# Optimization experiments

Measured on AMD Instinct MI355X. Metric: run time of the kernel, lower is better.

## Reference

```python
import jax, jax.numpy as jnp
from jax import lax
import numpy as np

BATCH = 8
FH, FW, A = 32, 256, 6            # feature map height/width, anchors per cell
TOTAL_ANCHORS = FH * FW * A       # 49152
PRE_NMS_TOPN = 2000
POST_NMS_TOPN = 300
NMS_IOU = 0.7
VARIANCES = np.array([0.1, 0.1, 0.2, 0.2], dtype=np.float32)


def _make_anchors():
    # Grid anchors, normalized [y1, x1, y2, x2], A scales/ratios per cell.
    cy = (np.arange(FH, dtype=np.float32) + 0.5) / FH
    cx = (np.arange(FW, dtype=np.float32) + 0.5) / FW
    sizes = np.array([0.02, 0.04, 0.08, 0.03, 0.06, 0.12], dtype=np.float32)  # A sizes
    ratios = np.array([1.0, 1.0, 1.0, 2.0, 0.5, 1.0], dtype=np.float32)
    h = sizes * np.sqrt(ratios)
    w = sizes / np.sqrt(ratios)
    CY, CX = np.meshgrid(cy, cx, indexing='ij')            # [FH, FW]
    CY = CY[:, :, None]; CX = CX[:, :, None]               # [FH, FW, 1]
    y1 = CY - 0.5 * h; x1 = CX - 0.5 * w
    y2 = CY + 0.5 * h; x2 = CX + 0.5 * w
    anc = np.stack([y1, x1, y2, x2], axis=-1).reshape(-1, 4)  # [TOTAL_ANCHORS, 4]
    return jnp.asarray(anc, dtype=jnp.float32)


def setup_inputs() -> dict:
    key = jax.random.key(0)
    k1, k2 = jax.random.split(key)
    rpn_bbox_deltas = jax.random.normal(k1, (BATCH, FH, FW, A * 4), dtype=jnp.float32)
    rpn_labels = jax.random.normal(k2, (BATCH, FH, FW, A), dtype=jnp.float32)
    return {
        'rpn_bbox_deltas': rpn_bbox_deltas,
        'rpn_labels': rpn_labels,
        'anchors': _make_anchors(),
    }


def _decode(anchors, deltas):
    # anchors [N,4] y1x1y2x2, deltas [B,N,4] (dy,dx,dh,dw)
    ah = anchors[:, 2] - anchors[:, 0]
    aw = anchors[:, 3] - anchors[:, 1]
    acy = anchors[:, 0] + 0.5 * ah
    acx = anchors[:, 1] + 0.5 * aw
    bh = jnp.exp(deltas[..., 2]) * ah
    bw = jnp.exp(deltas[..., 3]) * aw
    bcy = deltas[..., 0] * ah + acy
    bcx = deltas[..., 1] * aw + acx
    y1 = bcy - 0.5 * bh
    x1 = bcx - 0.5 * bw
    return jnp.stack([y1, x1, y1 + bh, x1 + bw], axis=-1)


def _pairwise_iou(boxes):
    # boxes [N,4] -> [N,N]
    y1, x1, y2, x2 = boxes[:, 0], boxes[:, 1], boxes[:, 2], boxes[:, 3]
    area = (y2 - y1) * (x2 - x1)
    iy1 = jnp.maximum(y1[:, None], y1[None, :])
    ix1 = jnp.maximum(x1[:, None], x1[None, :])
    iy2 = jnp.minimum(y2[:, None], y2[None, :])
    ix2 = jnp.minimum(x2[:, None], x2[None, :])
    inter = jnp.maximum(iy2 - iy1, 0.0) * jnp.maximum(ix2 - ix1, 0.0)
    union = area[:, None] + area[None, :] - inter
    return inter / jnp.maximum(union, 1e-8)


def _nms_single(boxes, scores):
    # boxes [P,4] sorted by score desc, scores [P] in [0,1]
    P = boxes.shape[0]
    ious = _pairwise_iou(boxes)
    idx = jnp.arange(P)

    def body(i, keep):
        sup = (ious[i] > NMS_IOU) & (idx > i) & keep[i]
        return keep & (~sup)

    keep = lax.fori_loop(0, P, body, jnp.ones((P,), dtype=bool))
    masked = jnp.where(keep, scores, -1.0)
    top_sc, top_idx = lax.top_k(masked, POST_NMS_TOPN)
    valid = top_sc >= 0.0
    out_boxes = jnp.clip(boxes[top_idx], 0.0, 1.0) * valid[:, None].astype(boxes.dtype)
    out_scores = jnp.where(valid, top_sc, 0.0)
    return out_boxes, out_scores


def reference(rpn_bbox_deltas, rpn_labels, anchors):
    B = rpn_bbox_deltas.shape[0]
    deltas = rpn_bbox_deltas.reshape(B, TOTAL_ANCHORS, 4)
    labels = jax.nn.softmax(rpn_labels, axis=-1).reshape(B, TOTAL_ANCHORS)
    deltas = deltas * jnp.asarray(VARIANCES)
    bboxes = _decode(anchors, deltas)                          # [B, N, 4]
    pre_scores, pre_idx = lax.top_k(labels, PRE_NMS_TOPN)      # [B, P]
    pre_boxes = jnp.take_along_axis(bboxes, pre_idx[:, :, None], axis=1)  # [B, P, 4]
    roi_boxes, roi_scores = jax.vmap(_nms_single)(pre_boxes, pre_scores)
    return (lax.stop_gradient(roi_boxes), lax.stop_gradient(roi_scores))
```

## Files before the change

### kernel.cpp

```cpp
#include <hip/hip_runtime.h>
#include <cstdint>
#include <cstddef>

#define BATCH 8
#define FHh   32
#define FWw   256
#define NA    6
#define NANCH (FHh * FWw * NA)
#define PRE_K 2000
#define POST_K 300
#define SEGS  192
#define CAND_CAP 4096
#define BIN_LO 0x3E2Au
#define SH_BASE 0x3E00u
#define SHBIN 512
#define RMAX_EP 20

typedef unsigned long long u64;

#define WS_SC   0
#define WS_HIST 1572864
#define WS_CUTV 3670016
#define WS_CAND 4194304
#define WS_CNT  7340032
#define WS_PB   7602176
#define WS_PS   7858176
#define WS_SUPP 8388608

__global__ __launch_bounds__(1024) void k_zero(uint4* __restrict__ hist4) {
    hist4[threadIdx.x] = make_uint4(0u, 0u, 0u, 0u);
}

__global__ void k_softhist(const float* __restrict__ labels, float* __restrict__ scores,
                           unsigned int* __restrict__ hist) {
    int pos = blockIdx.x * blockDim.x + threadIdx.x;
    if (pos >= BATCH * FHh * FWw) return;
    int b = pos / (FHh * FWw);
    const float2* in2 = (const float2*)(labels + (size_t)pos * NA);
    float v[NA];
    float2 p0 = in2[0], p1 = in2[1], p2 = in2[2];
    v[0] = p0.x; v[1] = p0.y; v[2] = p1.x; v[3] = p1.y; v[4] = p2.x; v[5] = p2.y;
    float m = v[0];
#pragma unroll
    for (int a = 1; a < NA; ++a) m = fmaxf(m, v[a]);
    float s = 0.0f;
#pragma unroll
    for (int a = 0; a < NA; ++a) { v[a] = expf(v[a] - m); s += v[a]; }
    float inv = 1.0f / s;
    float2* o2 = (float2*)(scores + (size_t)pos * NA);
    unsigned int* hb = hist + (size_t)b * SHBIN;
#pragma unroll
    for (int a = 0; a < NA; ++a) v[a] *= inv;
    o2[0] = make_float2(v[0], v[1]);
    o2[1] = make_float2(v[2], v[3]);
    o2[2] = make_float2(v[4], v[5]);
#pragma unroll
    for (int a = 0; a < NA; ++a) {
        unsigned int bin = __float_as_uint(v[a]) >> 16;
        if (bin >= BIN_LO) atomicAdd(&hb[bin - SH_BASE], 1u);
    }
}

__global__ __launch_bounds__(64) void k_sfx(unsigned int* __restrict__ hist,
                                            unsigned int* __restrict__ cutv) {
    const int b = blockIdx.x;
    const int t = threadIdx.x;
    unsigned int* h = hist + (size_t)b * SHBIN;
    const int blk0 = SHBIN - 8 * (t + 1);
    uint4 q0 = *(const uint4*)(h + blk0);
    uint4 q1 = *(const uint4*)(h + blk0 + 4);
    unsigned int hv[8] = {q0.x, q0.y, q0.z, q0.w, q1.x, q1.y, q1.z, q1.w};
    unsigned int s = hv[0] + hv[1] + hv[2] + hv[3] + hv[4] + hv[5] + hv[6] + hv[7];
    unsigned int inc = s;
#pragma unroll
    for (int d = 1; d < 64; d <<= 1) {
        unsigned int v = __shfl_up(inc, d);
        if (t >= d) inc += v;
    }
    unsigned int run = inc - s;
    unsigned int o[8];
#pragma unroll
    for (int g = 7; g >= 0; --g) { o[g] = run; run += hv[g]; }
#pragma unroll
    for (int g = 0; g < 8; ++g)
        if (o[g] < PRE_K && o[g] + hv[g] >= PRE_K)
            cutv[b * 16] = SH_BASE + (unsigned)(blk0 + g);
    uint4 w0 = make_uint4(o[0], o[1], o[2], o[3]);
    uint4 w1 = make_uint4(o[4], o[5], o[6], o[7]);
    *(uint4*)(h + blk0) = w0;
    *(uint4*)(h + blk0 + 4) = w1;
}

__global__ __launch_bounds__(256) void k_gather(
        const float* __restrict__ scores, const unsigned int* __restrict__ cutv,
        u64* __restrict__ cand, unsigned int* __restrict__ counts) {
    const int blk = blockIdx.x;
    const int b = blk / SEGS, kb = blk - b * SEGS;
    const int tid = threadIdx.x;
    __shared__ unsigned int s_cut;
    __shared__ unsigned int s_wcnt[4];
    if (tid == 0) s_cut = cutv[b * 16];
    __syncthreads();
    const int idx = kb * 256 + tid;
    const unsigned int bits = __float_as_uint(scores[(size_t)b * NANCH + idx]);
    const bool pass = (bits >> 16) >= s_cut;
    const u64 m = __ballot(pass);
    const int lane = tid & 63, w = tid >> 6;
    if (lane == 0) s_wcnt[w] = (unsigned int)__popcll(m);
    __syncthreads();
    unsigned int pre = 0, tot = 0;
#pragma unroll
    for (int i = 0; i < 4; ++i) { unsigned int c = s_wcnt[i]; if (i < w) pre += c; tot += c; }
    if (pass) {
        unsigned int rank = pre + (unsigned int)__popcll(m & ((1ull << lane) - 1ull));
        cand[((size_t)b * SEGS + kb) * 256 + rank] =
            ((u64)bits << 32) | (unsigned int)(~idx);
    }
    if (tid == 0) counts[b * SEGS + kb] = tot;
}

__global__ __launch_bounds__(1024) void k_rankdec(
        const u64* __restrict__ cand, const unsigned int* __restrict__ counts,
        const unsigned int* __restrict__ sfx,
        const float* __restrict__ deltas, const float* __restrict__ anchors,
        float4* __restrict__ pre_boxes, float* __restrict__ pre_scores) {
    const int b = blockIdx.x;
    const int tid = threadIdx.x;
    __shared__ u64 grouped[CAND_CAP];
    __shared__ unsigned int cursor[CAND_CAP];
    for (int i = tid; i < CAND_CAP; i += 1024) { grouped[i] = 0ull; cursor[i] = 0u; }
    __syncthreads();
    const unsigned int* sfb = sfx + (size_t)b * SHBIN;

    if (tid < SEGS) {
        unsigned int v = counts[b * SEGS + tid];
        const u64* seg = cand + ((size_t)b * SEGS + tid) * 256;
        for (unsigned int k = 0; k < v; ++k) {
            u64 key = seg[k];
            unsigned int bin = (unsigned int)(key >> 48) - SH_BASE;
            unsigned int g0 = sfb[bin];
            unsigned int slot = g0 + atomicAdd(&cursor[g0], 1u);
            if (slot < CAND_CAP) grouped[slot] = key;
        }
    }
    __syncthreads();

    for (int p = tid; p < CAND_CAP; p += 1024) {
        u64 key = grouped[p];
        if (key == 0ull) continue;
        unsigned int bin = (unsigned int)(key >> 48) - SH_BASE;
        unsigned int g0 = sfb[bin];
        unsigned int c = cursor[g0];
        unsigned int rank = g0;
        unsigned int qe = g0 + c; if (qe > CAND_CAP) qe = CAND_CAP;
        for (unsigned int q = g0; q < qe; ++q) rank += (grouped[q] > key);
        if (rank < PRE_K) {
            int idx = (int)(~(unsigned int)key);
            float score = __uint_as_float((unsigned int)(key >> 32));
            const float* anc = anchors + (size_t)idx * 4;
            const float* del = deltas + ((size_t)b * NANCH + idx) * 4;
            float a0 = anc[0], a1 = anc[1], a2 = anc[2], a3 = anc[3];
            float ah = a2 - a0, aw = a3 - a1;
            float acy = a0 + 0.5f * ah, acx = a1 + 0.5f * aw;
            float d0 = del[0] * 0.1f, d1 = del[1] * 0.1f;
            float d2 = del[2] * 0.2f, d3 = del[3] * 0.2f;
            float bh = expf(d2) * ah, bw = expf(d3) * aw;
            float bcy = d0 * ah + acy, bcx = d1 * aw + acx;
            float y1 = bcy - 0.5f * bh, x1 = bcx - 0.5f * bw;
            pre_boxes[(size_t)b * PRE_K + rank] = make_float4(y1, x1, y1 + bh, x1 + bw);
            pre_scores[(size_t)b * PRE_K + rank] = score;
        }
    }
}

__global__ __launch_bounds__(64) void k_iou(const float4* __restrict__ pre_boxes,
                                            u64* __restrict__ supp) {
    const int cb = blockIdx.x;
    const int rb = blockIdx.y;
    const int b  = blockIdx.z;
    const int lane = threadIdx.x;
    const int i = rb * 64 + lane;
    const int j0 = cb * 64;
    if (cb < rb) return;
    __shared__ float4 sbox[64];
    const float4* boxes = pre_boxes + (size_t)b * PRE_K;
    int j = j0 + lane;
    sbox[lane] = (j < PRE_K) ? boxes[j] : make_float4(0.f, 0.f, 0.f, 0.f);
    __syncthreads();
    if (i >= PRE_K) return;
    float4 bi = boxes[i];
    float area_i = (bi.z - bi.x) * (bi.w - bi.y);
    u64 bits = 0ull;
    const int tmax = (PRE_K - j0 < 64) ? (PRE_K - j0) : 64;
    for (int t = 0; t < tmax; ++t) {
        int jj = j0 + t;
        if (jj <= i) continue;
        float4 bj = sbox[t];
        float iy1 = fmaxf(bi.x, bj.x), ix1 = fmaxf(bi.y, bj.y);
        float iy2 = fminf(bi.z, bj.z), ix2 = fminf(bi.w, bj.w);
        float inter = fmaxf(iy2 - iy1, 0.0f) * fmaxf(ix2 - ix1, 0.0f);
        float area_j = (bj.z - bj.x) * (bj.w - bj.y);
        float uni = area_i + area_j - inter;
        float iou = inter / fmaxf(uni, 1e-8f);
        if (iou > 0.7f) bits |= (1ull << t);
    }
    supp[((size_t)b * PRE_K + i) * 32 + cb] = bits;
}

__device__ __forceinline__ u64 readlane64(u64 x, int ln) {
    unsigned int lo = __builtin_amdgcn_readlane((unsigned int)x, ln);
    unsigned int hi = __builtin_amdgcn_readlane((unsigned int)(x >> 32), ln);
    return ((u64)hi << 32) | (u64)lo;
}

template <int ROWS>
__device__ __forceinline__ u64 proc_epoch(const u64* __restrict__ bufp, int wi,
                                          int p, int w, u64& r0, u64& r1) {
    const u64 wmask = (w >= wi) ? ~0ull : 0ull;
    u64 acc = r0 | r1;
    u64 cur = ~(readlane64(acc, wi) | readlane64(acc, 32 + wi));
#pragma unroll
    for (int g = 0; g < ROWS / 16; ++g) {
        u64 ld[8];
#pragma unroll
        for (int k = 0; k < 8; ++k)
            ld[k] = bufp[(g * 16 + 2 * k + p) * 32 + w] & wmask;
        u64 t0 = (ld[0] | ld[1]) | (ld[2] | ld[3]);
        u64 t1 = (ld[4] | ld[5]) | (ld[6] | ld[7]);
        u64 tor = t0 | t1;
        u64 intra = readlane64(tor, wi) | readlane64(tor, 32 + wi);
        if (intra == 0ull) {
#pragma unroll
            for (int k = 0; k < 8; ++k) {
                int bitpos = g * 16 + 2 * k + p;
                u64 msk = ((cur >> bitpos) & 1ull) ? ~0ull : 0ull;
                if (k & 1) r1 |= ld[k] & msk; else r0 |= ld[k] & msk;
            }
        } else {
#pragma unroll
            for (int c = 0; c < 16; ++c) {
                const int pi = c & 1, k = c >> 1;
                if ((cur >> (g * 16 + c)) & 1ull) {
                    cur &= ~readlane64(ld[k], pi * 32 + wi);
                    u64 msk = (p == pi) ? ~0ull : 0ull;
                    if (k & 1) r1 |= ld[k] & msk; else r0 |= ld[k] & msk;
                }
            }
        }
    }
    return cur;
}

__device__ void fill_epoch(u64* __restrict__ dst, const float4* __restrict__ boxes,
                           int e, int l, int rows) {
    const int total = rows * 32;
    for (int idx = l; idx < total; idx += 64) {
        const int rl = idx >> 5, w = idx & 31;
        const int i = e * 64 + rl;
        const int j0 = w * 64;
        u64 bits = 0ull;
        if (i < PRE_K && j0 + 63 > i) {
            float4 bi = boxes[i];
            float area_i = (bi.z - bi.x) * (bi.w - bi.y);
            const int tmax = (PRE_K - j0 < 64) ? (PRE_K - j0) : 64;
            for (int t = 0; t < tmax; ++t) {
                int jj = j0 + t;
                if (jj <= i) continue;
                float4 bj = boxes[jj];
                float iy1 = fmaxf(bi.x, bj.x), ix1 = fmaxf(bi.y, bj.y);
                float iy2 = fminf(bi.z, bj.z), ix2 = fminf(bi.w, bj.w);
                float inter = fmaxf(iy2 - iy1, 0.0f) * fmaxf(ix2 - ix1, 0.0f);
                float area_j = (bj.z - bj.x) * (bj.w - bj.y);
                float uni = area_i + area_j - inter;
                float iou = inter / fmaxf(uni, 1e-8f);
                if (iou > 0.7f) bits |= (1ull << t);
            }
        }
        dst[idx] = bits;
    }
}

__global__ __launch_bounds__(64) void k_final(const u64* __restrict__ supp,
                        const float4* __restrict__ pre_boxes,
                        const float* __restrict__ pre_scores,
                        float* __restrict__ out) {
    const int b = blockIdx.x;
    const int l = threadIdx.x;
    const int p = l >> 5, w = l & 31;
    float* ob = out + (size_t)b * POST_K * 4;
    float* os = out + (size_t)BATCH * POST_K * 4 + (size_t)b * POST_K;
    for (int t = l; t < POST_K * 4; t += 64) ob[t] = 0.0f;
    for (int t = l; t < POST_K; t += 64) os[t] = 0.0f;
    asm volatile("s_waitcnt vmcnt(0)" ::: "memory");

    __shared__ u64 sbuf[3][2048];
    const char* Sb = (const char*)(supp + (size_t)b * PRE_K * 32);
    const float4* boxes = pre_boxes + (size_t)b * PRE_K;

#define ISSUE_EPOCH(ep)                                                       \
    do {                                                                      \
        const char* gsrc_ = Sb + (size_t)(ep) * 16384 + (size_t)l * 16;       \
        char* ldst_ = (char*)&sbuf[(ep) % 3][0];                              \
        _Pragma("unroll")                                                     \
        for (int k_ = 0; k_ < 16; ++k_)                                       \
            __builtin_amdgcn_global_load_lds(                                 \
                (const __attribute__((address_space(1))) void*)(gsrc_ + k_ * 1024), \
                (__attribute__((address_space(3))) void*)(ldst_ + k_ * 1024), \
                16, 0, 0);                                                    \
    } while (0)

    u64 r0 = 0ull, r1 = 0ull;
    int kept = 0;
    bool done = false;
    ISSUE_EPOCH(0);
    ISSUE_EPOCH(1);
    for (int e = 0; e <= RMAX_EP - 3; ++e) {
        ISSUE_EPOCH(e + 2);
        asm volatile("s_waitcnt vmcnt(32)" ::: "memory");
        __builtin_amdgcn_sched_barrier(0);
        u64 curf = proc_epoch<64>(&sbuf[e % 3][0], e, p, w, r0, r1);
        kept += __builtin_popcountll(curf);
        if (kept >= POST_K) { done = true; break; }
    }
    if (!done) {
        asm volatile("s_waitcnt vmcnt(16)" ::: "memory");
        __builtin_amdgcn_sched_barrier(0);
        u64 curf = proc_epoch<64>(&sbuf[(RMAX_EP - 2) % 3][0], RMAX_EP - 2, p, w, r0, r1);
        kept += __builtin_popcountll(curf);
        if (kept >= POST_K) done = true;
    }
    if (!done) {
        asm volatile("s_waitcnt vmcnt(0)" ::: "memory");
        __builtin_amdgcn_sched_barrier(0);
        u64 curf = proc_epoch<64>(&sbuf[(RMAX_EP - 1) % 3][0], RMAX_EP - 1, p, w, r0, r1);
        kept += __builtin_popcountll(curf);
        if (kept >= POST_K) done = true;
    }
    if (!done) {
        for (int e = RMAX_EP; e < 32; ++e) {
            fill_epoch(&sbuf[0][0], boxes, e, l, (e == 31) ? 16 : 64);
            __syncthreads();
            u64 curf;
            if (e < 31) curf = proc_epoch<64>(&sbuf[0][0], e, p, w, r0, r1);
            else        curf = proc_epoch<16>(&sbuf[0][0], e, p, w, r0, r1) & 0xFFFFull;
            kept += __builtin_popcountll(curf);
            if (kept >= POST_K) break;
            __syncthreads();
        }
    }
    asm volatile("s_waitcnt vmcnt(0)" ::: "memory");
#undef ISSUE_EPOCH

    u64 full = r0 | r1;
    u64 oth = __shfl(full, w + 32);
    u64 kw = ~(full | oth);
    if (w == 31) kw &= 0xFFFFull;
    int cnt = (l < 32) ? __builtin_popcountll(kw) : 0;
    int cum = cnt;
#pragma unroll
    for (int d = 1; d < 64; d <<= 1) {
        int v = __shfl_up(cum, d);
        if (l >= d) cum += v;
    }
    int r = cum - cnt;
    __syncthreads();
    if (l < 32) {
        u64 m = kw;
        while (m != 0ull && r < POST_K) {
            int t = __builtin_ctzll(m);
            m &= m - 1ull;
            int i = w * 64 + t;
            float4 bx = pre_boxes[(size_t)b * PRE_K + i];
            ob[r * 4 + 0] = fminf(fmaxf(bx.x, 0.0f), 1.0f);
            ob[r * 4 + 1] = fminf(fmaxf(bx.y, 0.0f), 1.0f);
            ob[r * 4 + 2] = fminf(fmaxf(bx.z, 0.0f), 1.0f);
            ob[r * 4 + 3] = fminf(fmaxf(bx.w, 0.0f), 1.0f);
            os[r] = pre_scores[(size_t)b * PRE_K + i];
            ++r;
        }
    }
}

extern "C" void kernel_launch(void* const* d_in, const int* in_sizes, int n_in,
                              void* d_out, int out_size, void* d_ws, size_t ws_size,
                              hipStream_t stream) {
    const float* deltas  = (const float*)d_in[0];
    const float* labels  = (const float*)d_in[1];
    const float* anchors = (const float*)d_in[2];
    float* out = (float*)d_out;

    char* ws = (char*)d_ws;
    float* scores          = (float*)(ws + WS_SC);
    unsigned int* hist     = (unsigned int*)(ws + WS_HIST);
    unsigned int* cutv     = (unsigned int*)(ws + WS_CUTV);
    u64* cd                = (u64*)(ws + WS_CAND);
    unsigned int* cntp     = (unsigned int*)(ws + WS_CNT);
    float4* pre_boxes      = (float4*)(ws + WS_PB);
    float* pre_scores      = (float*)(ws + WS_PS);
    u64* sp                = (u64*)(ws + WS_SUPP);

    k_zero<<<1, 1024, 0, stream>>>((uint4*)hist);
    k_softhist<<<(BATCH * FHh * FWw + 255) / 256, 256, 0, stream>>>(labels, scores, hist);
    k_sfx<<<BATCH, 64, 0, stream>>>(hist, cutv);
    k_gather<<<BATCH * SEGS, 256, 0, stream>>>(scores, cutv, cd, cntp);
    k_rankdec<<<BATCH, 1024, 0, stream>>>(cd, cntp, hist, deltas, anchors,
                                          pre_boxes, pre_scores);
    k_iou<<<dim3(32, RMAX_EP, BATCH), 64, 0, stream>>>(pre_boxes, sp);
    k_final<<<BATCH, 64, 0, stream>>>(sp, pre_boxes, pre_scores, out);
}
```

Before: 86.78 us.

## Fold histogram suffix scan into gather and rankdec; deepen final prefetch ring

Removes the separate suffix-scan kernel. Each gather block now scans the 512-bin histogram itself to find the cutoff bin, and the rank/decode kernel rebuilds the suffix offsets in shared memory. This saves one launch and its dependency stall at the cost of redundant scan work in every gather block. Separately, the final NMS kernel's async LDS prefetch ring grows from 3 to 5 buffers with four epochs in flight, giving more latency hiding in exchange for more LDS.

```diff
diff --git a/kernel.cpp b/kernel.cpp
--- a/kernel.cpp
+++ b/kernel.cpp
@@ -20,7 +20,6 @@
 
 #define WS_SC   0
 #define WS_HIST 1572864
-#define WS_CUTV 3670016
 #define WS_CAND 4194304
 #define WS_CNT  7340032
 #define WS_PB   7602176
@@ -61,51 +60,44 @@
     }
 }
 
-__global__ __launch_bounds__(64) void k_sfx(unsigned int* __restrict__ hist,
-                                            unsigned int* __restrict__ cutv) {
-    const int b = blockIdx.x;
-    const int t = threadIdx.x;
-    unsigned int* h = hist + (size_t)b * SHBIN;
-    const int blk0 = SHBIN - 8 * (t + 1);
-    uint4 q0 = *(const uint4*)(h + blk0);
-    uint4 q1 = *(const uint4*)(h + blk0 + 4);
-    unsigned int hv[8] = {q0.x, q0.y, q0.z, q0.w, q1.x, q1.y, q1.z, q1.w};
-    unsigned int s = hv[0] + hv[1] + hv[2] + hv[3] + hv[4] + hv[5] + hv[6] + hv[7];
-    unsigned int inc = s;
-#pragma unroll
-    for (int d = 1; d < 64; d <<= 1) {
-        unsigned int v = __shfl_up(inc, d);
-        if (t >= d) inc += v;
-    }
-    unsigned int run = inc - s;
-    unsigned int o[8];
-#pragma unroll
-    for (int g = 7; g >= 0; --g) { o[g] = run; run += hv[g]; }
-#pragma unroll
-    for (int g = 0; g < 8; ++g)
-        if (o[g] < PRE_K && o[g] + hv[g] >= PRE_K)
-            cutv[b * 16] = SH_BASE + (unsigned)(blk0 + g);
-    uint4 w0 = make_uint4(o[0], o[1], o[2], o[3]);
-    uint4 w1 = make_uint4(o[4], o[5], o[6], o[7]);
-    *(uint4*)(h + blk0) = w0;
-    *(uint4*)(h + blk0 + 4) = w1;
-}
-
 __global__ __launch_bounds__(256) void k_gather(
-        const float* __restrict__ scores, const unsigned int* __restrict__ cutv,
+        const float* __restrict__ scores, const unsigned int* __restrict__ hist,
         u64* __restrict__ cand, unsigned int* __restrict__ counts) {
     const int blk = blockIdx.x;
     const int b = blk / SEGS, kb = blk - b * SEGS;
     const int tid = threadIdx.x;
+    const int lane = tid & 63, w = tid >> 6;
+    __shared__ unsigned int s_wsum[4];
     __shared__ unsigned int s_cut;
     __shared__ unsigned int s_wcnt[4];
-    if (tid == 0) s_cut = cutv[b * 16];
-    __syncthreads();
+
+    const unsigned int* hb = hist + (size_t)b * SHBIN;
+    const int base = SHBIN - 2 * (tid + 1);
+    unsigned int hlo = hb[base], hhi = hb[base + 1];
+    unsigned int s = hlo + hhi;
+    unsigned int inc = s;
+#pragma unroll
+    for (int d = 1; d < 64; d <<= 1) {
+        unsigned int v = __shfl_up(inc, d);
+        if (lane >= d) inc += v;
+    }
+    if (lane == 63) s_wsum[w] = inc;
+    __syncthreads();
+    unsigned int woff = 0;
+#pragma unroll
+    for (int i = 0; i < 4; ++i) if (i < w) woff += s_wsum[i];
+    unsigned int excl = woff + inc - s;
+    if (excl < PRE_K && excl + s >= PRE_K) {
+        unsigned int run = excl + hhi;
+        s_cut = SH_BASE + (unsigned int)(run >= PRE_K ? base + 1 : base);
+    }
+    __syncthreads();
+    const unsigned int cutr = s_cut;
+
     const int idx = kb * 256 + tid;
     const unsigned int bits = __float_as_uint(scores[(size_t)b * NANCH + idx]);
-    const bool pass = (bits >> 16) >= s_cut;
+    const bool pass = (bits >> 16) >= cutr;
     const u64 m = __ballot(pass);
-    const int lane = tid & 63, w = tid >> 6;
     if (lane == 0) s_wcnt[w] = (unsigned int)__popcll(m);
     __syncthreads();
     unsigned int pre = 0, tot = 0;
@@ -121,16 +113,34 @@
 
 __global__ __launch_bounds__(1024) void k_rankdec(
         const u64* __restrict__ cand, const unsigned int* __restrict__ counts,
-        const unsigned int* __restrict__ sfx,
+        const unsigned int* __restrict__ hist,
         const float* __restrict__ deltas, const float* __restrict__ anchors,
         float4* __restrict__ pre_boxes, float* __restrict__ pre_scores) {
     const int b = blockIdx.x;
     const int tid = threadIdx.x;
+    const int lane = tid & 63, wid = tid >> 6;
     __shared__ u64 grouped[CAND_CAP];
     __shared__ unsigned int cursor[CAND_CAP];
+    __shared__ unsigned int sfx_lds[SHBIN];
+    __shared__ unsigned int s_ws8[8];
     for (int i = tid; i < CAND_CAP; i += 1024) { grouped[i] = 0ull; cursor[i] = 0u; }
-    __syncthreads();
-    const unsigned int* sfb = sfx + (size_t)b * SHBIN;
+
+    unsigned int c = (tid < SHBIN) ? hist[(size_t)b * SHBIN + (SHBIN - 1 - tid)] : 0u;
+    unsigned int inc = c;
+#pragma unroll
+    for (int d = 1; d < 64; d <<= 1) {
+        unsigned int v = __shfl_up(inc, d);
+        if (lane >= d) inc += v;
+    }
+    if (lane == 63 && wid < 8) s_ws8[wid] = inc;
+    __syncthreads();
+    if (tid < SHBIN) {
+        unsigned int woff = 0;
+#pragma unroll
+        for (int i = 0; i < 8; ++i) if (i < wid) woff += s_ws8[i];
+        sfx_lds[SHBIN - 1 - tid] = woff + inc - c;
+    }
+    __syncthreads();
 
     if (tid < SEGS) {
         unsigned int v = counts[b * SEGS + tid];
@@ -138,7 +148,7 @@
         for (unsigned int k = 0; k < v; ++k) {
             u64 key = seg[k];
             unsigned int bin = (unsigned int)(key >> 48) - SH_BASE;
-            unsigned int g0 = sfb[bin];
+            unsigned int g0 = sfx_lds[bin];
             unsigned int slot = g0 + atomicAdd(&cursor[g0], 1u);
             if (slot < CAND_CAP) grouped[slot] = key;
         }
@@ -149,10 +159,10 @@
         u64 key = grouped[p];
         if (key == 0ull) continue;
         unsigned int bin = (unsigned int)(key >> 48) - SH_BASE;
-        unsigned int g0 = sfb[bin];
-        unsigned int c = cursor[g0];
+        unsigned int g0 = sfx_lds[bin];
+        unsigned int cg = cursor[g0];
         unsigned int rank = g0;
-        unsigned int qe = g0 + c; if (qe > CAND_CAP) qe = CAND_CAP;
+        unsigned int qe = g0 + cg; if (qe > CAND_CAP) qe = CAND_CAP;
         for (unsigned int q = g0; q < qe; ++q) rank += (grouped[q] > key);
         if (rank < PRE_K) {
             int idx = (int)(~(unsigned int)key);
@@ -293,14 +303,14 @@
     for (int t = l; t < POST_K; t += 64) os[t] = 0.0f;
     asm volatile("s_waitcnt vmcnt(0)" ::: "memory");
 
-    __shared__ u64 sbuf[3][2048];
+    __shared__ u64 sbuf[5][2048];
     const char* Sb = (const char*)(supp + (size_t)b * PRE_K * 32);
     const float4* boxes = pre_boxes + (size_t)b * PRE_K;
 
 #define ISSUE_EPOCH(ep)                                                       \
     do {                                                                      \
         const char* gsrc_ = Sb + (size_t)(ep) * 16384 + (size_t)l * 16;       \
-        char* ldst_ = (char*)&sbuf[(ep) % 3][0];                              \
+        char* ldst_ = (char*)&sbuf[(ep) % 5][0];                              \
         _Pragma("unroll")                                                     \
         for (int k_ = 0; k_ < 16; ++k_)                                       \
             __builtin_amdgcn_global_load_lds(                                 \
@@ -314,28 +324,20 @@
     bool done = false;
     ISSUE_EPOCH(0);
     ISSUE_EPOCH(1);
-    for (int e = 0; e <= RMAX_EP - 3; ++e) {
-        ISSUE_EPOCH(e + 2);
-        asm volatile("s_waitcnt vmcnt(32)" ::: "memory");
+    ISSUE_EPOCH(2);
+    ISSUE_EPOCH(3);
+    for (int e = 0; e < RMAX_EP; ++e) {
+        if (e <= RMAX_EP - 4)      asm volatile("s_waitcnt vmcnt(48)" ::: "memory");
+        else if (e == RMAX_EP - 3) asm volatile("s_waitcnt vmcnt(32)" ::: "memory");
+        else if (e == RMAX_EP - 2) asm volatile("s_waitcnt vmcnt(16)" ::: "memory");
+        else                       asm volatile("s_waitcnt vmcnt(0)"  ::: "memory");
         __builtin_amdgcn_sched_barrier(0);
-        u64 curf = proc_epoch<64>(&sbuf[e % 3][0], e, p, w, r0, r1);
+        if (e + 4 < RMAX_EP) ISSUE_EPOCH(e + 4);
+        u64 curf = proc_epoch<64>(&sbuf[e % 5][0], e, p, w, r0, r1);
         kept += __builtin_popcountll(curf);
         if (kept >= POST_K) { done = true; break; }
     }
-    if (!done) {
-        asm volatile("s_waitcnt vmcnt(16)" ::: "memory");
-        __builtin_amdgcn_sched_barrier(0);
-        u64 curf = proc_epoch<64>(&sbuf[(RMAX_EP - 2) % 3][0], RMAX_EP - 2, p, w, r0, r1);
-        kept += __builtin_popcountll(curf);
-        if (kept >= POST_K) done = true;
-    }
-    if (!done) {
-        asm volatile("s_waitcnt vmcnt(0)" ::: "memory");
-        __builtin_amdgcn_sched_barrier(0);
-        u64 curf = proc_epoch<64>(&sbuf[(RMAX_EP - 1) % 3][0], RMAX_EP - 1, p, w, r0, r1);
-        kept += __builtin_popcountll(curf);
-        if (kept >= POST_K) done = true;
-    }
+    asm volatile("s_waitcnt vmcnt(0)" ::: "memory");
     if (!done) {
         for (int e = RMAX_EP; e < 32; ++e) {
             fill_epoch(&sbuf[0][0], boxes, e, l, (e == 31) ? 16 : 64);
@@ -348,7 +350,6 @@
             __syncthreads();
         }
     }
-    asm volatile("s_waitcnt vmcnt(0)" ::: "memory");
 #undef ISSUE_EPOCH
 
     u64 full = r0 | r1;
@@ -392,7 +393,6 @@
     char* ws = (char*)d_ws;
     float* scores          = (float*)(ws + WS_SC);
     unsigned int* hist     = (unsigned int*)(ws + WS_HIST);
-    unsigned int* cutv     = (unsigned int*)(ws + WS_CUTV);
     u64* cd                = (u64*)(ws + WS_CAND);
     unsigned int* cntp     = (unsigned int*)(ws + WS_CNT);
     float4* pre_boxes      = (float4*)(ws + WS_PB);
@@ -401,8 +401,7 @@
 
     k_zero<<<1, 1024, 0, stream>>>((uint4*)hist);
     k_softhist<<<(BATCH * FHh * FWw + 255) / 256, 256, 0, stream>>>(labels, scores, hist);
-    k_sfx<<<BATCH, 64, 0, stream>>>(hist, cutv);
-    k_gather<<<BATCH * SEGS, 256, 0, stream>>>(scores, cutv, cd, cntp);
+    k_gather<<<BATCH * SEGS, 256, 0, stream>>>(scores, hist, cd, cntp);
     k_rankdec<<<BATCH, 1024, 0, stream>>>(cd, cntp, hist, deltas, anchors,
                                           pre_boxes, pre_scores);
     k_iou<<<dim3(32, RMAX_EP, BATCH), 64, 0, stream>>>(pre_boxes, sp);
```

Result: no change. 87.13 us (+0.4%).
